# Optimization experiments

Measured on AMD Instinct MI355X. Metric: run time of the kernel, lower is better.

## Reference

```python
import jax, jax.numpy as jnp
import numpy as np

B, M, K = 4096, 64, 3          # graphs, points per graph, knn k
FX, FP = 59, 3                 # node features, position dims (FX+FP = 62)
EPS = 1e-5


def _lin_init(key, fan_in, fan_out):
    k1, k2 = jax.random.split(key)
    s = 1.0 / np.sqrt(fan_in)
    W = jax.random.uniform(k1, (fan_in, fan_out), jnp.float32, -s, s)
    b = jax.random.uniform(k2, (fan_out,), jnp.float32, -s, s)
    return W, b


def setup_inputs() -> dict:
    key = jax.random.key(0)
    ks = jax.random.split(key, 8)
    x = jax.random.normal(ks[0], (B * M, FX), jnp.float32)
    pos = jax.random.normal(ks[1], (B * M, FP), jnp.float32)
    batch = jnp.repeat(jnp.arange(B, dtype=jnp.int32), M)
    W1, b1 = _lin_init(ks[2], FX + FP, 128)
    W2, b2 = _lin_init(ks[3], 128, 128)
    Wc1, bc1 = _lin_init(ks[4], 128, 256)
    Wc2, bc2 = _lin_init(ks[5], 256, 1)
    return dict(
        x=x, pos=pos, batch=batch,
        W1=W1, b1=b1, g1=jnp.ones(128), be1=jnp.zeros(128),
        W2=W2, b2=b2, g2=jnp.ones(128), be2=jnp.zeros(128),
        Wc1=Wc1, bc1=bc1, gc1=jnp.ones(256), bec1=jnp.zeros(256),
        Wc2=Wc2, bc2=bc2, gc2=jnp.ones(1), bec2=jnp.zeros(1),
    )


def _mlp_block(h, W, b, g, be):
    # Linear -> ReLU -> BatchNorm1d (training-mode batch statistics)
    h = jax.nn.relu(h @ W + b)
    mu = h.mean(axis=0)
    var = h.var(axis=0)  # biased, as torch BN uses for normalization
    return g * (h - mu) * jax.lax.rsqrt(var + EPS) + be


def _knn_idx(pos_b):
    # pos_b: [B, M, FP]; per-graph k-NN (loop=False)
    d = jnp.sum((pos_b[:, :, None, :] - pos_b[:, None, :, :]) ** 2, axis=-1)  # [B,M,M]
    d = d + jnp.eye(M, dtype=d.dtype) * 1e10  # exclude self-loops
    _, nbr = jax.lax.top_k(-d, K)  # [B, M, K] neighbor (source) indices
    return nbr


def reference(x, pos, batch, W1, b1, g1, be1, W2, b2, g2, be2,
              Wc1, bc1, gc1, bec1, Wc2, bc2, gc2, bec2):
    x_b = x.reshape(B, M, FX)
    pos_b = pos.reshape(B, M, FP)
    nbr = _knn_idx(pos_b)                                   # [B,M,K]
    # gather neighbor features and relative positions (edge messages)
    xj = jax.vmap(lambda xb, nb: xb[nb])(x_b, nbr)          # [B,M,K,FX]
    pj = jax.vmap(lambda pb, nb: pb[nb])(pos_b, nbr)        # [B,M,K,FP]
    rel = pj - pos_b[:, :, None, :]
    msg = jnp.concatenate([xj, rel], axis=-1).reshape(B * M * K, FX + FP)
    # local_nn on every edge, then max aggregation per target node
    h = _mlp_block(msg, W1, b1, g1, be1)                    # [E,128]
    h = h.reshape(B, M, K, 128).max(axis=2).reshape(B * M, 128)
    # global_nn per node
    h = _mlp_block(h, W2, b2, g2, be2)                      # [N,128]
    # global mean pool over graphs
    sums = jax.ops.segment_sum(h, batch, num_segments=B)
    cnt = jax.ops.segment_sum(jnp.ones((B * M,), h.dtype), batch, num_segments=B)
    pooled = sums / cnt[:, None]                            # [B,128]
    # classifier MLP([128,256,1])
    c = _mlp_block(pooled, Wc1, bc1, gc1, bec1)
    c = _mlp_block(c, Wc2, bc2, gc2, bec2)                  # [B,1]
    return jax.nn.sigmoid(c)[:, 0]
```

## Files before the change

### kernel.cpp

```cpp
#include <hip/hip_runtime.h>
#include <hip/hip_bf16.h>
#include <math.h>

#define NB   4096
#define MM   64
#define KNN  3
#define FX   59
#define H    128
#define NN   (NB*MM)
#define NE   (NN*KNN)
#define C1   256
#define EPSB 1e-5f
#define NSH  16

typedef __attribute__((ext_vector_type(8))) short short8;
typedef __attribute__((ext_vector_type(4))) float f32x4;

__device__ __forceinline__ float wave_red(float v) {
#pragma unroll
    for (int m = 32; m >= 1; m >>= 1) v += __shfl_xor(v, m, 64);
    return v;
}

__device__ __forceinline__ void atomAddF(float* p, float v) {
    __hip_atomic_fetch_add(p, v, __ATOMIC_RELAXED, __HIP_MEMORY_SCOPE_AGENT);
}

__device__ __forceinline__ unsigned short f2bf(float f) {
    union { float f; unsigned u; } v; v.f = f;
    unsigned r = v.u + 0x7fffu + ((v.u >> 16) & 1u);
    return (unsigned short)(r >> 16);
}

__device__ __forceinline__ unsigned int pack_bf2(float a, float b) {
    union { __hip_bfloat162 h; unsigned int u; } cv;
    cv.h = __float22bfloat162_rn(make_float2(a, b));
    return cv.u;
}

__global__ __launch_bounds__(512, 8) void k_knn_mfma1(
    const float* __restrict__ x, const float* __restrict__ pos,
    const float* __restrict__ W1, const float* __restrict__ b1,
    unsigned short* __restrict__ h1max,
    float* __restrict__ S1sh, float* __restrict__ Q1sh)
{
    __shared__ float pos_s[MM * 3];
    __shared__ int   nbr_s[MM * 3];
    __shared__ float b1_s[H];
    __shared__ float w1p_s[3 * H];
    __shared__ __align__(16) unsigned short a_s[MM * 72];
    __shared__ __align__(16) unsigned int   u_s32[MM * 66];

    const int blk = blockIdx.x, tid = threadIdx.x;
    const float* xg = x + (size_t)blk * MM * FX;
    const float* pg = pos + (size_t)blk * MM * 3;

    {
        const int node = tid >> 3, c0g = (tid & 7) * 8;
        unsigned short vals[8];
#pragma unroll
        for (int i = 0; i < 8; ++i) {
            int c = c0g + i;
            float v = (c < FX) ? xg[node * FX + c]
                               : ((c < 62) ? pg[node * 3 + (c - FX)] : 0.f);
            vals[i] = f2bf(v);
        }
        *(short8*)(a_s + node * 72 + c0g) = *(short8*)&vals[0];
    }
    if (tid < MM * 3) pos_s[tid] = pg[tid];
    if (tid < H) b1_s[tid] = b1[tid];
    if (tid < 3 * H) w1p_s[tid] = W1[(FX + (tid >> 7)) * H + (tid & 127)];

    const int lane = tid & 63;
    const int w    = tid >> 6;
    const int m    = lane & 15;
    const int kg   = lane >> 4;
    const int ch   = w * 16 + m;

    short8 bfr[2];
#pragma unroll
    for (int kc = 0; kc < 2; ++kc) {
        unsigned short t8[8];
#pragma unroll
        for (int i = 0; i < 8; ++i) {
            int k = kc * 32 + kg * 8 + i;
            t8[i] = (k < 62) ? f2bf(W1[k * H + ch]) : (unsigned short)0;
        }
        bfr[kc] = *(short8*)t8;
    }
    __syncthreads();

    {
        const int node = tid >> 3, q = tid & 7;
        const float px = pos_s[node * 3 + 0];
        const float py = pos_s[node * 3 + 1];
        const float pz = pos_s[node * 3 + 2];
        float d0 = 1e30f, d1 = 1e30f, d2 = 1e30f;
        int   i0 = 1 << 30, i1 = 1 << 30, i2 = 1 << 30;
        for (int jj = 0; jj < 8; ++jj) {
            int j = q * 8 + jj;
            if (j == node) continue;
            float dx = pos_s[j * 3 + 0] - px;
            float dy = pos_s[j * 3 + 1] - py;
            float dz = pos_s[j * 3 + 2] - pz;
            float d = dx * dx + dy * dy + dz * dz;
            bool b2v = (d < d2) || (d == d2 && j < i2);
            bool b1v = (d < d1) || (d == d1 && j < i1);
            bool b0v = (d < d0) || (d == d0 && j < i0);
            float nd2 = b1v ? d1 : d; int ni2 = b1v ? i1 : j;
            float nd1 = b0v ? d0 : d; int ni1 = b0v ? i0 : j;
            d2 = b2v ? nd2 : d2; i2 = b2v ? ni2 : i2;
            d1 = b1v ? nd1 : d1; i1 = b1v ? ni1 : i1;
            d0 = b0v ? d   : d0; i0 = b0v ? j   : i0;
        }
#pragma unroll
        for (int mq = 1; mq <= 4; mq <<= 1) {
            float e[3]; int f[3];
            e[0] = __shfl_xor(d0, mq, 64); f[0] = __shfl_xor(i0, mq, 64);
            e[1] = __shfl_xor(d1, mq, 64); f[1] = __shfl_xor(i1, mq, 64);
            e[2] = __shfl_xor(d2, mq, 64); f[2] = __shfl_xor(i2, mq, 64);
#pragma unroll
            for (int t3 = 0; t3 < 3; ++t3) {
                float ev = e[t3]; int fv = f[t3];
                bool b2v = (ev < d2) || (ev == d2 && fv < i2);
                bool b1v = (ev < d1) || (ev == d1 && fv < i1);
                bool b0v = (ev < d0) || (ev == d0 && fv < i0);
                float nd2 = b1v ? d1 : ev; int ni2 = b1v ? i1 : fv;
                float nd1 = b0v ? d0 : ev; int ni1 = b0v ? i0 : fv;
                d2 = b2v ? nd2 : d2; i2 = b2v ? ni2 : i2;
                d1 = b1v ? nd1 : d1; i1 = b1v ? ni1 : i1;
                d0 = b0v ? ev  : d0; i0 = b0v ? fv  : i0;
            }
        }
        if (q == 0) {
            nbr_s[node * 3 + 0] = i0;
            nbr_s[node * 3 + 1] = i1;
            nbr_s[node * 3 + 2] = i2;
        }
    }

    f32x4 acc[4];
#pragma unroll
    for (int rt = 0; rt < 4; ++rt) acc[rt] = (f32x4){0.f, 0.f, 0.f, 0.f};

#pragma unroll
    for (int kc = 0; kc < 2; ++kc)
#pragma unroll
        for (int rt = 0; rt < 4; ++rt) {
            short8 a = *(const short8*)(a_s + (rt * 16 + m) * 72 + kc * 32 + kg * 8);
            acc[rt] = __builtin_amdgcn_mfma_f32_16x16x32_bf16(bfr[kc], a, acc[rt], 0, 0, 0);
        }
#pragma unroll
    for (int rt = 0; rt < 4; ++rt) {
        int node = rt * 16 + m;
        int pidx = 8 * w + 2 * kg;
        uint2 val;
        val.x = pack_bf2(acc[rt][0], acc[rt][1]);
        val.y = pack_bf2(acc[rt][2], acc[rt][3]);
        *(uint2*)(u_s32 + node * 66 + pidx) = val;
    }
    __syncthreads();

    const int c0 = 2 * lane, c1v = 2 * lane + 1;
    const float wpa0 = w1p_s[c0],      wpa1 = w1p_s[H + c0],  wpa2 = w1p_s[2 * H + c0];
    const float wpb0 = w1p_s[c1v],     wpb1 = w1p_s[H + c1v], wpb2 = w1p_s[2 * H + c1v];
    const float b1a = b1_s[c0], b1b = b1_s[c1v];
    float s0 = 0.f, s1 = 0.f, q0 = 0.f, q1 = 0.f;
    unsigned int* hout32 = (unsigned int*)(h1max + (size_t)blk * MM * H);
#pragma unroll
    for (int ii = 0; ii < 8; ++ii) {
        int node = w * 8 + ii;
        int j0 = nbr_s[node * 3 + 0];
        int j1 = nbr_s[node * 3 + 1];
        int j2 = nbr_s[node * 3 + 2];
        float px = pos_s[node * 3 + 0], py = pos_s[node * 3 + 1], pz = pos_s[node * 3 + 2];
        float basea = b1a - (px * wpa0 + py * wpa1 + pz * wpa2);
        float baseb = b1b - (px * wpb0 + py * wpb1 + pz * wpb2);
        unsigned int v0 = u_s32[j0 * 66 + lane];
        unsigned int v1 = u_s32[j1 * 66 + lane];
        unsigned int v2 = u_s32[j2 * 66 + lane];
        float h0a = fmaxf(__uint_as_float(v0 << 16) + basea, 0.f);
        float h1a = fmaxf(__uint_as_float(v1 << 16) + basea, 0.f);
        float h2a = fmaxf(__uint_as_float(v2 << 16) + basea, 0.f);
        float h0b = fmaxf(__uint_as_float(v0 & 0xffff0000u) + baseb, 0.f);
        float h1b = fmaxf(__uint_as_float(v1 & 0xffff0000u) + baseb, 0.f);
        float h2b = fmaxf(__uint_as_float(v2 & 0xffff0000u) + baseb, 0.f);
        s0 += h0a + h1a + h2a; q0 += h0a * h0a + h1a * h1a + h2a * h2a;
        s1 += h0b + h1b + h2b; q1 += h0b * h0b + h1b * h1b + h2b * h2b;
        float ma = fmaxf(fmaxf(h0a, h1a), h2a);
        float mb = fmaxf(fmaxf(h0b, h1b), h2b);
        hout32[node * 64 + lane] = pack_bf2(ma, mb);
    }
    __syncthreads();

    float* s_red = (float*)a_s;
    float* q_red = (float*)u_s32;
    *(float2*)(s_red + w * 128 + c0) = make_float2(s0, s1);
    *(float2*)(q_red + w * 128 + c0) = make_float2(q0, q1);
    __syncthreads();
    const int sel = blk & (NSH - 1);
    if (tid < 128) {
        float S = 0.f;
#pragma unroll
        for (int ww = 0; ww < 8; ++ww) S += s_red[ww * 128 + tid];
        atomAddF(&S1sh[sel * H + tid], S);
    } else if (tid < 256) {
        int t2 = tid - 128;
        float Q = 0.f;
#pragma unroll
        for (int ww = 0; ww < 8; ++ww) Q += q_red[ww * 128 + t2];
        atomAddF(&Q1sh[sel * H + t2], Q);
    }
}

__global__ __launch_bounds__(128) void k_prep2(
    const float* __restrict__ W2, const float* __restrict__ S1sh,
    const float* __restrict__ Q1sh, const float* __restrict__ g1,
    const float* __restrict__ be1, const float* __restrict__ b2,
    unsigned short* __restrict__ W2t, float* __restrict__ b2p)
{
    const int n = blockIdx.x, k = threadIdx.x;
    float S = 0.f, Q = 0.f;
#pragma unroll
    for (int i = 0; i < NSH; ++i) { S += S1sh[i * H + k]; Q += Q1sh[i * H + k]; }
    float mu  = S * (1.f / (float)NE);
    float var = Q * (1.f / (float)NE) - mu * mu;
    float a   = g1[k] * rsqrtf(var + EPSB);
    float cc  = be1[k] - mu * a;
    float wv  = W2[k * H + n];
    W2t[n * H + k] = f2bf(a * wv);
    float contrib = wave_red(cc * wv);
    __shared__ float red2[2];
    if ((k & 63) == 0) red2[k >> 6] = contrib;
    __syncthreads();
    if (k == 0) b2p[n] = b2[n] + red2[0] + red2[1];
}

__global__ __launch_bounds__(256) void k_mfma2(
    const unsigned short* __restrict__ h1max, const unsigned short* __restrict__ W2t,
    const float* __restrict__ b2p,
    float* __restrict__ graphsum, float* __restrict__ S2sh, float* __restrict__ Q2sh)
{
    __shared__ __align__(16) unsigned short a_s[MM * 136];
    const int blk = blockIdx.x, tid = threadIdx.x;
    const unsigned short* hg = h1max + (size_t)blk * MM * H;
    for (int t = tid; t < MM * H / 8; t += 256) {
        int row = t >> 4, col8 = (t & 15) * 8;
        *(short8*)(a_s + row * 136 + col8) = *(const short8*)(hg + row * H + col8);
    }
    __syncthreads();

    const int lane = tid & 63, w = tid >> 6, wcol = w * 32;
    const int m = lane & 15, kg = lane >> 4;

    short8 bfr[2][4];
#pragma unroll
    for (int ct = 0; ct < 2; ++ct)
#pragma unroll
        for (int kc = 0; kc < 4; ++kc)
            bfr[ct][kc] = *(const short8*)(W2t + (wcol + ct * 16 + m) * H + kc * 32 + kg * 8);

    f32x4 acc[4][2];
#pragma unroll
    for (int rt = 0; rt < 4; ++rt)
#pragma unroll
        for (int ct = 0; ct < 2; ++ct) acc[rt][ct] = (f32x4){0.f, 0.f, 0.f, 0.f};

#pragma unroll
    for (int kc = 0; kc < 4; ++kc)
#pragma unroll
        for (int rt = 0; rt < 4; ++rt) {
            short8 a = *(const short8*)(a_s + (rt * 16 + m) * 136 + kc * 32 + kg * 8);
#pragma unroll
            for (int ct = 0; ct < 2; ++ct)
                acc[rt][ct] = __builtin_amdgcn_mfma_f32_16x16x32_bf16(a, bfr[ct][kc], acc[rt][ct], 0, 0, 0);
        }

    const int sel = blk & (NSH - 1);
#pragma unroll
    for (int ct = 0; ct < 2; ++ct) {
        float bv = b2p[wcol + ct * 16 + m];
        float s = 0.f, q = 0.f;
#pragma unroll
        for (int rt = 0; rt < 4; ++rt)
#pragma unroll
            for (int r = 0; r < 4; ++r) {
                float v = fmaxf(acc[rt][ct][r] + bv, 0.f);
                s += v; q += v * v;
            }
        s += __shfl_xor(s, 16, 64); q += __shfl_xor(q, 16, 64);
        s += __shfl_xor(s, 32, 64); q += __shfl_xor(q, 32, 64);
        if (lane < 16) {
            int col = wcol + ct * 16 + lane;
            graphsum[(size_t)blk * H + col] = s;
            atomAddF(&S2sh[sel * H + col], s);
            atomAddF(&Q2sh[sel * H + col], q);
        }
    }
}

__global__ __launch_bounds__(256) void k_cls1(
    const float* __restrict__ graphsum,
    const float* __restrict__ S2sh, const float* __restrict__ Q2sh,
    const float* __restrict__ g2, const float* __restrict__ be2,
    const float* __restrict__ Wc1, const float* __restrict__ bc1,
    float* __restrict__ c1raw, float* __restrict__ S3, float* __restrict__ Q3)
{
    __shared__ float a2_s[H], c2_s[H];
    const int blk = blockIdx.x, tid = threadIdx.x;
    if (tid < H) {
        float S = 0.f, Q = 0.f;
#pragma unroll
        for (int i = 0; i < NSH; ++i) { S += S2sh[i * H + tid]; Q += Q2sh[i * H + tid]; }
        float mu  = S * (1.f / (float)NN);
        float var = Q * (1.f / (float)NN) - mu * mu;
        float a   = g2[tid] * rsqrtf(var + EPSB);
        a2_s[tid] = a;
        c2_s[tid] = be2[tid] - mu * a;
    }
    __syncthreads();
    __shared__ float pooled_s[16 * H];
    const int g0 = blk * 16;
    for (int t = tid; t < 16 * H; t += 256) {
        int f = t & 127;
        pooled_s[t] = a2_s[f] * (graphsum[(size_t)g0 * H + t] * (1.f / 64.f)) + c2_s[f];
    }
    __syncthreads();
    const int c = tid;
    float acc[16];
    const float bias = bc1[c];
#pragma unroll
    for (int gi = 0; gi < 16; ++gi) acc[gi] = bias;
    for (int f = 0; f < H; ++f) {
        float wv = Wc1[f * C1 + c];
#pragma unroll
        for (int gi = 0; gi < 16; ++gi) acc[gi] += pooled_s[gi * H + f] * wv;
    }
    float s = 0.f, q = 0.f;
#pragma unroll
    for (int gi = 0; gi < 16; ++gi) {
        float h = fmaxf(acc[gi], 0.f);
        c1raw[(size_t)(g0 + gi) * C1 + c] = h;
        s += h; q += h * h;
    }
    atomAddF(&S3[c], s);
    atomAddF(&Q3[c], q);
}

__global__ __launch_bounds__(256) void k_cls2(
    const float* __restrict__ c1raw,
    const float* __restrict__ S3, const float* __restrict__ Q3,
    const float* __restrict__ gc1, const float* __restrict__ bec1,
    const float* __restrict__ Wc2, const float* __restrict__ bc2,
    float* __restrict__ z, float* __restrict__ SzQz)
{
    __shared__ float a3_s[C1], c3_s[C1], w3_s[C1];
    __shared__ float zloc[16];
    const int blk = blockIdx.x, tid = threadIdx.x;
    {
        float S = S3[tid], Q = Q3[tid];
        float mu  = S * (1.f / (float)NB);
        float var = Q * (1.f / (float)NB) - mu * mu;
        float a   = gc1[tid] * rsqrtf(var + EPSB);
        a3_s[tid] = a;
        c3_s[tid] = bec1[tid] - mu * a;
        w3_s[tid] = Wc2[tid];
    }
    __syncthreads();
    const int g0 = blk * 16;
    {
        const int gi = tid >> 4, part = tid & 15;
        const float* crow = c1raw + (size_t)(g0 + gi) * C1 + part * 16;
        float acc3 = 0.f;
#pragma unroll
        for (int i = 0; i < 16; i += 4) {
            float4 cv = *(const float4*)(crow + i);
            int f = part * 16 + i;
            acc3 += (a3_s[f + 0] * cv.x + c3_s[f + 0]) * w3_s[f + 0];
            acc3 += (a3_s[f + 1] * cv.y + c3_s[f + 1]) * w3_s[f + 1];
            acc3 += (a3_s[f + 2] * cv.z + c3_s[f + 2]) * w3_s[f + 2];
            acc3 += (a3_s[f + 3] * cv.w + c3_s[f + 3]) * w3_s[f + 3];
        }
#pragma unroll
        for (int mm = 1; mm <= 8; mm <<= 1) acc3 += __shfl_xor(acc3, mm, 64);
        if (part == 0) zloc[gi] = fmaxf(acc3 + bc2[0], 0.f);
    }
    __syncthreads();
    if (tid < 16) z[g0 + tid] = zloc[tid];
    if (tid == 0) {
        float s = 0.f, q = 0.f;
#pragma unroll
        for (int i = 0; i < 16; ++i) { float zz = zloc[i]; s += zz; q += zz * zz; }
        atomAddF(&SzQz[0], s);
        atomAddF(&SzQz[1], q);
    }
}

__global__ __launch_bounds__(256) void k_final(
    const float* __restrict__ z, const float* __restrict__ SzQz,
    const float* __restrict__ gc2, const float* __restrict__ bec2,
    float* __restrict__ out)
{
    const int g = blockIdx.x * 256 + threadIdx.x;
    float S = SzQz[0], Q = SzQz[1];
    float mu  = S * (1.f / 4096.f);
    float var = Q * (1.f / 4096.f) - mu * mu;
    float a   = gc2[0] * rsqrtf(var + EPSB);
    float cb  = bec2[0] - mu * a;
    float v = a * z[g] + cb;
    out[g] = 1.f / (1.f + expf(-v));
}

extern "C" void kernel_launch(void* const* d_in, const int* in_sizes, int n_in,
                              void* d_out, int out_size, void* d_ws, size_t ws_size,
                              hipStream_t stream)
{
    const float* x    = (const float*)d_in[0];
    const float* pos  = (const float*)d_in[1];
    const float* W1   = (const float*)d_in[3];
    const float* b1   = (const float*)d_in[4];
    const float* g1   = (const float*)d_in[5];
    const float* be1  = (const float*)d_in[6];
    const float* W2   = (const float*)d_in[7];
    const float* b2   = (const float*)d_in[8];
    const float* g2   = (const float*)d_in[9];
    const float* be2  = (const float*)d_in[10];
    const float* Wc1  = (const float*)d_in[11];
    const float* bc1  = (const float*)d_in[12];
    const float* gc1  = (const float*)d_in[13];
    const float* bec1 = (const float*)d_in[14];
    const float* Wc2  = (const float*)d_in[15];
    const float* bc2  = (const float*)d_in[16];
    const float* gc2  = (const float*)d_in[17];
    const float* bec2 = (const float*)d_in[18];
    float* out = (float*)d_out;

    float* ws = (float*)d_ws;
    size_t off = 0;
    auto alloc = [&](size_t n) { float* p = ws + off; off += n; return p; };
    unsigned short* h1max = (unsigned short*)alloc((size_t)NN * H / 2);
    unsigned short* W2t   = (unsigned short*)alloc(128 * 128 / 2);
    float* b2p     = alloc(H);
    float* graphsum= alloc((size_t)NB * H);
    float* c1raw   = alloc((size_t)NB * C1);
    float* zbuf    = alloc(NB);
    const size_t ATOMN = (size_t)4 * NSH * H + 2 * C1 + 2;
    float* atomics = alloc(ATOMN);
    float* S1sh = atomics;
    float* Q1sh = S1sh + NSH * H;
    float* S2sh = Q1sh + NSH * H;
    float* Q2sh = S2sh + NSH * H;
    float* S3   = Q2sh + NSH * H;
    float* Q3   = S3 + C1;
    float* SzQz = Q3 + C1;

    hipMemsetAsync(atomics, 0, ATOMN * sizeof(float), stream);
    k_knn_mfma1<<<dim3(NB), dim3(512), 0, stream>>>(x, pos, W1, b1, h1max, S1sh, Q1sh);
    k_prep2<<<dim3(128), dim3(128), 0, stream>>>(W2, S1sh, Q1sh, g1, be1, b2, W2t, b2p);
    k_mfma2<<<dim3(NB), dim3(256), 0, stream>>>(h1max, W2t, b2p, graphsum, S2sh, Q2sh);
    k_cls1<<<dim3(256), dim3(256), 0, stream>>>(graphsum, S2sh, Q2sh, g2, be2, Wc1, bc1, c1raw, S3, Q3);
    k_cls2<<<dim3(256), dim3(256), 0, stream>>>(c1raw, S3, Q3, gc1, bec1, Wc2, bc2, zbuf, SzQz);
    k_final<<<dim3(16), dim3(256), 0, stream>>>(zbuf, SzQz, gc2, bec2, out);
}
```

Measured before the change: 241.0 us.

## Fuse BN1 folding into mfma2 and merge classifier kernels via grid barriers

Removes k_prep2 by having each k_mfma2 block recompute the BN1 scale/shift and fold it into W2 on the fly. Each block now handles two graphs with 512 threads. The three classifier kernels become one, which uses atomic-counter grid barriers so the batch statistics are available without extra launches or round trips through global memory. The aim is to cut launch overhead and intermediate buffers. In exchange, every block redundantly reads W2 and the shard sums, and the spin barriers assume all 256 blocks are resident at once.

```diff
diff --git a/kernel.cpp b/kernel.cpp
--- a/kernel.cpp
+++ b/kernel.cpp
@@ -24,12 +24,6 @@
 
 __device__ __forceinline__ void atomAddF(float* p, float v) {
     __hip_atomic_fetch_add(p, v, __ATOMIC_RELAXED, __HIP_MEMORY_SCOPE_AGENT);
-}
-
-__device__ __forceinline__ unsigned short f2bf(float f) {
-    union { float f; unsigned u; } v; v.f = f;
-    unsigned r = v.u + 0x7fffu + ((v.u >> 16) & 1u);
-    return (unsigned short)(r >> 16);
 }
 
 __device__ __forceinline__ unsigned int pack_bf2(float a, float b) {
@@ -57,15 +51,17 @@
 
     {
         const int node = tid >> 3, c0g = (tid & 7) * 8;
-        unsigned short vals[8];
+        float v[8];
 #pragma unroll
         for (int i = 0; i < 8; ++i) {
-            int c = c0g + i;
-            float v = (c < FX) ? xg[node * FX + c]
-                               : ((c < 62) ? pg[node * 3 + (c - FX)] : 0.f);
-            vals[i] = f2bf(v);
-        }
-        *(short8*)(a_s + node * 72 + c0g) = *(short8*)&vals[0];
+            int cI = c0g + i;
+            v[i] = (cI < FX) ? xg[node * FX + cI]
+                             : ((cI < 62) ? pg[node * 3 + (cI - FX)] : 0.f);
+        }
+        uint4 pk;
+        pk.x = pack_bf2(v[0], v[1]); pk.y = pack_bf2(v[2], v[3]);
+        pk.z = pack_bf2(v[4], v[5]); pk.w = pack_bf2(v[6], v[7]);
+        *(uint4*)(a_s + node * 72 + c0g) = pk;
     }
     if (tid < MM * 3) pos_s[tid] = pg[tid];
     if (tid < H) b1_s[tid] = b1[tid];
@@ -80,13 +76,16 @@
     short8 bfr[2];
 #pragma unroll
     for (int kc = 0; kc < 2; ++kc) {
-        unsigned short t8[8];
+        float t8[8];
 #pragma unroll
         for (int i = 0; i < 8; ++i) {
             int k = kc * 32 + kg * 8 + i;
-            t8[i] = (k < 62) ? f2bf(W1[k * H + ch]) : (unsigned short)0;
-        }
-        bfr[kc] = *(short8*)t8;
+            t8[i] = (k < 62) ? W1[k * H + ch] : 0.f;
+        }
+        uint4 pk;
+        pk.x = pack_bf2(t8[0], t8[1]); pk.y = pack_bf2(t8[2], t8[3]);
+        pk.z = pack_bf2(t8[4], t8[5]); pk.w = pack_bf2(t8[6], t8[7]);
+        bfr[kc] = *(short8*)&pk;
     }
     __syncthreads();
 
@@ -213,53 +212,65 @@
     }
 }
 
-__global__ __launch_bounds__(128) void k_prep2(
-    const float* __restrict__ W2, const float* __restrict__ S1sh,
-    const float* __restrict__ Q1sh, const float* __restrict__ g1,
-    const float* __restrict__ be1, const float* __restrict__ b2,
-    unsigned short* __restrict__ W2t, float* __restrict__ b2p)
-{
-    const int n = blockIdx.x, k = threadIdx.x;
-    float S = 0.f, Q = 0.f;
-#pragma unroll
-    for (int i = 0; i < NSH; ++i) { S += S1sh[i * H + k]; Q += Q1sh[i * H + k]; }
-    float mu  = S * (1.f / (float)NE);
-    float var = Q * (1.f / (float)NE) - mu * mu;
-    float a   = g1[k] * rsqrtf(var + EPSB);
-    float cc  = be1[k] - mu * a;
-    float wv  = W2[k * H + n];
-    W2t[n * H + k] = f2bf(a * wv);
-    float contrib = wave_red(cc * wv);
-    __shared__ float red2[2];
-    if ((k & 63) == 0) red2[k >> 6] = contrib;
-    __syncthreads();
-    if (k == 0) b2p[n] = b2[n] + red2[0] + red2[1];
-}
-
-__global__ __launch_bounds__(256) void k_mfma2(
-    const unsigned short* __restrict__ h1max, const unsigned short* __restrict__ W2t,
-    const float* __restrict__ b2p,
+__global__ __launch_bounds__(512, 2) void k_mfma2(
+    const unsigned short* __restrict__ h1max, const float* __restrict__ W2,
+    const float* __restrict__ S1sh, const float* __restrict__ Q1sh,
+    const float* __restrict__ g1, const float* __restrict__ be1,
+    const float* __restrict__ b2,
     float* __restrict__ graphsum, float* __restrict__ S2sh, float* __restrict__ Q2sh)
 {
-    __shared__ __align__(16) unsigned short a_s[MM * 136];
+    __shared__ __align__(16) unsigned short a_s[2 * MM * 136];
+    __shared__ float af_s[H], cf_s[H];
     const int blk = blockIdx.x, tid = threadIdx.x;
-    const unsigned short* hg = h1max + (size_t)blk * MM * H;
-    for (int t = tid; t < MM * H / 8; t += 256) {
+    const unsigned short* hg = h1max + (size_t)blk * 2 * MM * H;
+
+    if (tid < H) {
+        float S = 0.f, Q = 0.f;
+#pragma unroll
+        for (int i = 0; i < NSH; ++i) { S += S1sh[i * H + tid]; Q += Q1sh[i * H + tid]; }
+        float mu  = S * (1.f / (float)NE);
+        float var = Q * (1.f / (float)NE) - mu * mu;
+        float a   = g1[tid] * rsqrtf(var + EPSB);
+        af_s[tid] = a;
+        cf_s[tid] = be1[tid] - mu * a;
+    }
+    for (int t = tid; t < 128 * 16; t += 512) {
         int row = t >> 4, col8 = (t & 15) * 8;
         *(short8*)(a_s + row * 136 + col8) = *(const short8*)(hg + row * H + col8);
     }
     __syncthreads();
 
-    const int lane = tid & 63, w = tid >> 6, wcol = w * 32;
+    const int lane = tid & 63, w = tid >> 6;
+    const int wg = w >> 2, wcol = (w & 3) * 32;
     const int m = lane & 15, kg = lane >> 4;
 
     short8 bfr[2][4];
-#pragma unroll
-    for (int ct = 0; ct < 2; ++ct)
-#pragma unroll
-        for (int kc = 0; kc < 4; ++kc)
-            bfr[ct][kc] = *(const short8*)(W2t + (wcol + ct * 16 + m) * H + kc * 32 + kg * 8);
-
+    float bp[2];
+#pragma unroll
+    for (int ct = 0; ct < 2; ++ct) {
+        const int n = wcol + ct * 16 + m;
+        float bsum = 0.f;
+#pragma unroll
+        for (int kc = 0; kc < 4; ++kc) {
+            float tt[8];
+#pragma unroll
+            for (int i = 0; i < 8; ++i) {
+                int k = kc * 32 + kg * 8 + i;
+                float wv = W2[k * H + n];
+                tt[i] = af_s[k] * wv;
+                bsum += cf_s[k] * wv;
+            }
+            uint4 pk;
+            pk.x = pack_bf2(tt[0], tt[1]); pk.y = pack_bf2(tt[2], tt[3]);
+            pk.z = pack_bf2(tt[4], tt[5]); pk.w = pack_bf2(tt[6], tt[7]);
+            bfr[ct][kc] = *(short8*)&pk;
+        }
+        bsum += __shfl_xor(bsum, 16, 64);
+        bsum += __shfl_xor(bsum, 32, 64);
+        bp[ct] = b2[n] + bsum;
+    }
+
+    const unsigned short* ar = a_s + wg * MM * 136;
     f32x4 acc[4][2];
 #pragma unroll
     for (int rt = 0; rt < 4; ++rt)
@@ -270,16 +281,17 @@
     for (int kc = 0; kc < 4; ++kc)
 #pragma unroll
         for (int rt = 0; rt < 4; ++rt) {
-            short8 a = *(const short8*)(a_s + (rt * 16 + m) * 136 + kc * 32 + kg * 8);
+            short8 a = *(const short8*)(ar + (rt * 16 + m) * 136 + kc * 32 + kg * 8);
 #pragma unroll
             for (int ct = 0; ct < 2; ++ct)
                 acc[rt][ct] = __builtin_amdgcn_mfma_f32_16x16x32_bf16(a, bfr[ct][kc], acc[rt][ct], 0, 0, 0);
         }
 
-    const int sel = blk & (NSH - 1);
+    const int gidx = blk * 2 + wg;
+    const int sel  = gidx & (NSH - 1);
 #pragma unroll
     for (int ct = 0; ct < 2; ++ct) {
-        float bv = b2p[wcol + ct * 16 + m];
+        float bv = bp[ct];
         float s = 0.f, q = 0.f;
 #pragma unroll
         for (int rt = 0; rt < 4; ++rt)
@@ -292,22 +304,33 @@
         s += __shfl_xor(s, 32, 64); q += __shfl_xor(q, 32, 64);
         if (lane < 16) {
             int col = wcol + ct * 16 + lane;
-            graphsum[(size_t)blk * H + col] = s;
+            graphsum[(size_t)gidx * H + col] = s;
             atomAddF(&S2sh[sel * H + col], s);
             atomAddF(&Q2sh[sel * H + col], q);
         }
     }
 }
 
-__global__ __launch_bounds__(256) void k_cls1(
+__global__ __launch_bounds__(256) void k_tail2(
     const float* __restrict__ graphsum,
     const float* __restrict__ S2sh, const float* __restrict__ Q2sh,
     const float* __restrict__ g2, const float* __restrict__ be2,
     const float* __restrict__ Wc1, const float* __restrict__ bc1,
-    float* __restrict__ c1raw, float* __restrict__ S3, float* __restrict__ Q3)
+    const float* __restrict__ gc1, const float* __restrict__ bec1,
+    const float* __restrict__ Wc2, const float* __restrict__ bc2,
+    const float* __restrict__ gc2, const float* __restrict__ bec2,
+    float* __restrict__ S3, float* __restrict__ Q3,
+    float* __restrict__ SzQz, int* __restrict__ cnts,
+    float* __restrict__ out)
 {
     __shared__ float a2_s[H], c2_s[H];
+    __shared__ float pooled_s[16 * H];
+    __shared__ float c1_s[16][C1 + 4];
+    __shared__ float a3_s[C1], c3_s[C1], w3_s[C1];
+    __shared__ float zloc[16];
     const int blk = blockIdx.x, tid = threadIdx.x;
+    const int g0 = blk * 16;
+
     if (tid < H) {
         float S = 0.f, Q = 0.f;
 #pragma unroll
@@ -319,46 +342,43 @@
         c2_s[tid] = be2[tid] - mu * a;
     }
     __syncthreads();
-    __shared__ float pooled_s[16 * H];
-    const int g0 = blk * 16;
     for (int t = tid; t < 16 * H; t += 256) {
         int f = t & 127;
         pooled_s[t] = a2_s[f] * (graphsum[(size_t)g0 * H + t] * (1.f / 64.f)) + c2_s[f];
     }
     __syncthreads();
-    const int c = tid;
-    float acc[16];
-    const float bias = bc1[c];
-#pragma unroll
-    for (int gi = 0; gi < 16; ++gi) acc[gi] = bias;
-    for (int f = 0; f < H; ++f) {
-        float wv = Wc1[f * C1 + c];
-#pragma unroll
-        for (int gi = 0; gi < 16; ++gi) acc[gi] += pooled_s[gi * H + f] * wv;
-    }
-    float s = 0.f, q = 0.f;
-#pragma unroll
-    for (int gi = 0; gi < 16; ++gi) {
-        float h = fmaxf(acc[gi], 0.f);
-        c1raw[(size_t)(g0 + gi) * C1 + c] = h;
-        s += h; q += h * h;
-    }
-    atomAddF(&S3[c], s);
-    atomAddF(&Q3[c], q);
-}
-
-__global__ __launch_bounds__(256) void k_cls2(
-    const float* __restrict__ c1raw,
-    const float* __restrict__ S3, const float* __restrict__ Q3,
-    const float* __restrict__ gc1, const float* __restrict__ bec1,
-    const float* __restrict__ Wc2, const float* __restrict__ bc2,
-    float* __restrict__ z, float* __restrict__ SzQz)
-{
-    __shared__ float a3_s[C1], c3_s[C1], w3_s[C1];
-    __shared__ float zloc[16];
-    const int blk = blockIdx.x, tid = threadIdx.x;
+
     {
-        float S = S3[tid], Q = Q3[tid];
+        const int c = tid;
+        float acc[16];
+        const float bias = bc1[c];
+#pragma unroll
+        for (int gi = 0; gi < 16; ++gi) acc[gi] = bias;
+        for (int f = 0; f < H; ++f) {
+            float wv = Wc1[f * C1 + c];
+#pragma unroll
+            for (int gi = 0; gi < 16; ++gi) acc[gi] += pooled_s[gi * H + f] * wv;
+        }
+        float s = 0.f, q = 0.f;
+#pragma unroll
+        for (int gi = 0; gi < 16; ++gi) {
+            float h = fmaxf(acc[gi], 0.f);
+            c1_s[gi][c] = h;
+            s += h; q += h * h;
+        }
+        atomAddF(&S3[c], s);
+        atomAddF(&Q3[c], q);
+    }
+    __syncthreads();
+    if (tid == 0) {
+        __hip_atomic_fetch_add(&cnts[0], 1, __ATOMIC_ACQ_REL, __HIP_MEMORY_SCOPE_AGENT);
+        while (__hip_atomic_load(&cnts[0], __ATOMIC_ACQUIRE, __HIP_MEMORY_SCOPE_AGENT) < 256) {}
+    }
+    __syncthreads();
+
+    {
+        float S = __hip_atomic_load(&S3[tid], __ATOMIC_RELAXED, __HIP_MEMORY_SCOPE_AGENT);
+        float Q = __hip_atomic_load(&Q3[tid], __ATOMIC_RELAXED, __HIP_MEMORY_SCOPE_AGENT);
         float mu  = S * (1.f / (float)NB);
         float var = Q * (1.f / (float)NB) - mu * mu;
         float a   = gc1[tid] * rsqrtf(var + EPSB);
@@ -367,15 +387,14 @@
         w3_s[tid] = Wc2[tid];
     }
     __syncthreads();
-    const int g0 = blk * 16;
+
     {
         const int gi = tid >> 4, part = tid & 15;
-        const float* crow = c1raw + (size_t)(g0 + gi) * C1 + part * 16;
         float acc3 = 0.f;
 #pragma unroll
         for (int i = 0; i < 16; i += 4) {
-            float4 cv = *(const float4*)(crow + i);
             int f = part * 16 + i;
+            float4 cv = *(const float4*)&c1_s[gi][f];
             acc3 += (a3_s[f + 0] * cv.x + c3_s[f + 0]) * w3_s[f + 0];
             acc3 += (a3_s[f + 1] * cv.y + c3_s[f + 1]) * w3_s[f + 1];
             acc3 += (a3_s[f + 2] * cv.z + c3_s[f + 2]) * w3_s[f + 2];
@@ -386,29 +405,27 @@
         if (part == 0) zloc[gi] = fmaxf(acc3 + bc2[0], 0.f);
     }
     __syncthreads();
-    if (tid < 16) z[g0 + tid] = zloc[tid];
     if (tid == 0) {
         float s = 0.f, q = 0.f;
 #pragma unroll
         for (int i = 0; i < 16; ++i) { float zz = zloc[i]; s += zz; q += zz * zz; }
         atomAddF(&SzQz[0], s);
         atomAddF(&SzQz[1], q);
-    }
-}
-
-__global__ __launch_bounds__(256) void k_final(
-    const float* __restrict__ z, const float* __restrict__ SzQz,
-    const float* __restrict__ gc2, const float* __restrict__ bec2,
-    float* __restrict__ out)
-{
-    const int g = blockIdx.x * 256 + threadIdx.x;
-    float S = SzQz[0], Q = SzQz[1];
-    float mu  = S * (1.f / 4096.f);
-    float var = Q * (1.f / 4096.f) - mu * mu;
-    float a   = gc2[0] * rsqrtf(var + EPSB);
-    float cb  = bec2[0] - mu * a;
-    float v = a * z[g] + cb;
-    out[g] = 1.f / (1.f + expf(-v));
+        __hip_atomic_fetch_add(&cnts[1], 1, __ATOMIC_ACQ_REL, __HIP_MEMORY_SCOPE_AGENT);
+        while (__hip_atomic_load(&cnts[1], __ATOMIC_ACQUIRE, __HIP_MEMORY_SCOPE_AGENT) < 256) {}
+    }
+    __syncthreads();
+
+    if (tid < 16) {
+        float S = __hip_atomic_load(&SzQz[0], __ATOMIC_RELAXED, __HIP_MEMORY_SCOPE_AGENT);
+        float Q = __hip_atomic_load(&SzQz[1], __ATOMIC_RELAXED, __HIP_MEMORY_SCOPE_AGENT);
+        float mu  = S * (1.f / 4096.f);
+        float var = Q * (1.f / 4096.f) - mu * mu;
+        float a   = gc2[0] * rsqrtf(var + EPSB);
+        float cb  = bec2[0] - mu * a;
+        float v = a * zloc[tid] + cb;
+        out[g0 + tid] = 1.f / (1.f + expf(-v));
+    }
 }
 
 extern "C" void kernel_launch(void* const* d_in, const int* in_sizes, int n_in,
@@ -439,12 +456,8 @@
     size_t off = 0;
     auto alloc = [&](size_t n) { float* p = ws + off; off += n; return p; };
     unsigned short* h1max = (unsigned short*)alloc((size_t)NN * H / 2);
-    unsigned short* W2t   = (unsigned short*)alloc(128 * 128 / 2);
-    float* b2p     = alloc(H);
-    float* graphsum= alloc((size_t)NB * H);
-    float* c1raw   = alloc((size_t)NB * C1);
-    float* zbuf    = alloc(NB);
-    const size_t ATOMN = (size_t)4 * NSH * H + 2 * C1 + 2;
+    float* graphsum = alloc((size_t)NB * H);
+    const size_t ATOMN = (size_t)4 * NSH * H + 2 * C1 + 2 + 2;
     float* atomics = alloc(ATOMN);
     float* S1sh = atomics;
     float* Q1sh = S1sh + NSH * H;
@@ -453,12 +466,13 @@
     float* S3   = Q2sh + NSH * H;
     float* Q3   = S3 + C1;
     float* SzQz = Q3 + C1;
+    int*   cnts = (int*)(SzQz + 2);
 
     hipMemsetAsync(atomics, 0, ATOMN * sizeof(float), stream);
     k_knn_mfma1<<<dim3(NB), dim3(512), 0, stream>>>(x, pos, W1, b1, h1max, S1sh, Q1sh);
-    k_prep2<<<dim3(128), dim3(128), 0, stream>>>(W2, S1sh, Q1sh, g1, be1, b2, W2t, b2p);
-    k_mfma2<<<dim3(NB), dim3(256), 0, stream>>>(h1max, W2t, b2p, graphsum, S2sh, Q2sh);
-    k_cls1<<<dim3(256), dim3(256), 0, stream>>>(graphsum, S2sh, Q2sh, g2, be2, Wc1, bc1, c1raw, S3, Q3);
-    k_cls2<<<dim3(256), dim3(256), 0, stream>>>(c1raw, S3, Q3, gc1, bec1, Wc2, bc2, zbuf, SzQz);
-    k_final<<<dim3(16), dim3(256), 0, stream>>>(zbuf, SzQz, gc2, bec2, out);
-}
+    k_mfma2<<<dim3(NB / 2), dim3(512), 0, stream>>>(h1max, W2, S1sh, Q1sh, g1, be1, b2,
+                                                    graphsum, S2sh, Q2sh);
+    k_tail2<<<dim3(256), dim3(256), 0, stream>>>(graphsum, S2sh, Q2sh, g2, be2,
+                                                 Wc1, bc1, gc1, bec1, Wc2, bc2, gc2, bec2,
+                                                 S3, Q3, SzQz, cnts, out);
+}
```

Result: slower. 263.4 us (+9.3%).
